# Performance work log

Hardware: AMD Instinct MI355X
Metric: run time of the kernel (lower is better)

The kernel has to match this reference:

```python
import jax, jax.numpy as jnp
import numpy as np
import math

B, Q, D = 1, 1024, 4096
H, KV, HD = 32, 8, 128
GROUP_FACTOR, LABEL_BITS, HEAVY_CONST = 8, 4, 256
ROPE_THETA = 10000.0
NEG = jnp.finfo(jnp.float32).min


def setup_inputs() -> dict:
    key = jax.random.key(0)
    ks = jax.random.split(key, 5)
    hidden_states = jax.random.normal(ks[0], (B, Q, D), jnp.float32)
    Wq = jax.random.normal(ks[1], (D, H * HD), jnp.float32) * 0.02
    Wk = jax.random.normal(ks[2], (D, KV * HD), jnp.float32) * 0.02
    Wv = jax.random.normal(ks[3], (D, KV * HD), jnp.float32) * 0.02
    Wo = jax.random.normal(ks[4], (H * HD, D), jnp.float32) * 0.02
    # additive causal mask [B,1,Q,Q]
    causal = jnp.tril(jnp.ones((Q, Q), bool))
    attention_mask = jnp.where(causal, 0.0, NEG)[None, None].astype(jnp.float32)
    position_ids = jnp.arange(Q, dtype=jnp.int64 if jax.config.jax_enable_x64 else jnp.int32)[None]
    # per-head channel permutation (sorted channel importance order)
    rng = np.random.default_rng(0)
    sorted_channel = jnp.asarray(np.stack([rng.permutation(HD) for _ in range(H)]), jnp.int32)
    return {"hidden_states": hidden_states, "attention_mask": attention_mask,
            "position_ids": position_ids, "Wq": Wq, "Wk": Wk, "Wv": Wv, "Wo": Wo,
            "sorted_channel": sorted_channel}


def pseudo_quantize(t, q_bit):
    max_quant = 2 ** q_bit - 1
    mn = jnp.min(t, axis=-1, keepdims=True)
    mx = jnp.max(t, axis=-1, keepdims=True)
    rng = mx - mn
    rng = jnp.where(rng == 0, 1.0, rng)
    scale = max_quant / rng
    quant = jnp.clip(jnp.round((t - mn) * scale), 0, max_quant)
    return quant / scale + mn


def rotate_half(x):
    x1, x2 = jnp.split(x, 2, axis=-1)
    return jnp.concatenate([-x2, x1], axis=-1)


def _forward(hidden_states, attention_mask, Wq, Wk, Wv, Wo, position_ids, sorted_channel):
    bsz, q_len, _ = hidden_states.shape
    q = (hidden_states @ Wq).reshape(bsz, q_len, H, HD).transpose(0, 2, 1, 3)   # [B,H,Q,HD]
    k = (hidden_states @ Wk).reshape(bsz, q_len, KV, HD).transpose(0, 2, 1, 3)  # [B,KV,Q,HD]
    v = (hidden_states @ Wv).reshape(bsz, q_len, KV, HD).transpose(0, 2, 1, 3)
    kv_len = q_len

    # RoPE
    inv_freq = 1.0 / (ROPE_THETA ** (jnp.arange(0, HD, 2, dtype=jnp.float32) / HD))
    freqs = position_ids.astype(jnp.float32)[..., None] * inv_freq  # [B,Q,HD/2]
    emb = jnp.concatenate([freqs, freqs], axis=-1)
    cos = jnp.cos(emb)[:, None]  # [B,1,Q,HD]
    sin = jnp.sin(emb)[:, None]
    q = q * cos + rotate_half(q) * sin
    k = k * cos + rotate_half(k) * sin
    prev_q = q  # upper_layer_embedding is None -> previous_query_states == query_states

    # GQA repeat
    groups = H // KV
    k = jnp.repeat(k, groups, axis=1)  # [B,H,K,HD]
    v = jnp.repeat(v, groups, axis=1)

    attn = jnp.einsum('bhqd,bhkd->bhqk', q, k) / math.sqrt(HD)

    # channel gather per head (sorted_channel: [H,HD] permutation)
    idx = jnp.broadcast_to(sorted_channel[None, :, None, :], q.shape)
    sq = jnp.take_along_axis(prev_q, idx, axis=-1)
    sk = jnp.take_along_axis(k, jnp.broadcast_to(sorted_channel[None, :, None, :], k.shape), axis=-1)
    outlier = HD // GROUP_FACTOR
    gq = sq[..., :outlier]
    gk = sk[..., :outlier]
    if LABEL_BITS < 16:
        gq = pseudo_quantize(gq, LABEL_BITS)
        gk = pseudo_quantize(gk, LABEL_BITS)
    gattn = jnp.einsum('bhqd,bhkd->bhqk', gq, gk) / math.sqrt(outlier)

    attn = attn + attention_mask
    gattn = gattn + attention_mask

    # keep top heavy_const positions per query by grouped score (descending)
    rank = jnp.argsort(jnp.argsort(-gattn, axis=-1), axis=-1)
    attn = jnp.where(rank < HEAVY_CONST, attn, -jnp.inf)

    w = jax.nn.softmax(attn.astype(jnp.float32), axis=-1).astype(v.dtype)
    out = jnp.einsum('bhqk,bhkd->bhqd', w, v)
    out = out.transpose(0, 2, 1, 3).reshape(bsz, q_len, H * HD)
    return out @ Wo


def reference(hidden_states, attention_mask, position_ids, Wq, Wk, Wv, Wo, sorted_channel):
    return _forward(hidden_states, attention_mask, Wq, Wk, Wv, Wo, position_ids, sorted_channel)
```

## Files before the change

### kernel.cpp

```cpp
#include <hip/hip_runtime.h>
#include <hip/hip_bf16.h>
#include <math.h>


typedef __hip_bfloat16 bf16;
typedef unsigned short ushort_t;
typedef __attribute__((ext_vector_type(8))) short short8;
typedef __attribute__((ext_vector_type(4))) float f32x4;
typedef __attribute__((ext_vector_type(4))) unsigned u32x4;

#define QL   1024
#define DM   4096
#define NH   32
#define NKV  8
#define GRP  4
#define HD   128
#define OUTL 16
#define HC   256
#define MNEG (-1.0e30f)

__device__ __forceinline__ unsigned mapf(float f) {
  unsigned u = __float_as_uint(f);
  return (u & 0x80000000u) ? ~u : (u | 0x80000000u);
}

__device__ __forceinline__ unsigned short f2bf(float x) {
  unsigned u = __float_as_uint(x);
  unsigned r = (u + 0x7FFFu + ((u >> 16) & 1u)) >> 16;
  return (unsigned short)r;
}
__device__ __forceinline__ float bf2f(unsigned short h) {
  return __uint_as_float(((unsigned)h) << 16);
}

__device__ __forceinline__ void split8(const float* p, short8& h, short8& l) {
  f32x4 a = *(const f32x4*)p;
  f32x4 b = *(const f32x4*)(p + 4);
#pragma unroll
  for (int i = 0; i < 4; i++) {
    unsigned short hh = f2bf(a[i]);
    h[i] = (short)hh;
    l[i] = (short)f2bf(a[i] - bf2f(hh));
  }
#pragma unroll
  for (int i = 0; i < 4; i++) {
    unsigned short hh = f2bf(b[i]);
    h[4 + i] = (short)hh;
    l[4 + i] = (short)f2bf(b[i] - bf2f(hh));
  }
}

__device__ __forceinline__ void splitp8(const float* p, unsigned* o) {
  f32x4 a = *(const f32x4*)p;
  f32x4 b = *(const f32x4*)(p + 4);
#pragma unroll
  for (int i = 0; i < 4; i++) {
    unsigned short hh = f2bf(a[i]);
    unsigned short ll = f2bf(a[i] - bf2f(hh));
    o[i] = (unsigned)hh | ((unsigned)ll << 16);
  }
#pragma unroll
  for (int i = 0; i < 4; i++) {
    unsigned short hh = f2bf(b[i]);
    unsigned short ll = f2bf(b[i] - bf2f(hh));
    o[4 + i] = (unsigned)hh | ((unsigned)ll << 16);
  }
}

__device__ __forceinline__ int aswz(int r, int k) {
  return r * 32 + (k ^ (((r >> 1) & 3) << 3));
}

__device__ __forceinline__ void gll16(const bf16* g, bf16* l) {
  __builtin_amdgcn_global_load_lds(
      (const __attribute__((address_space(1))) void*)g,
      (__attribute__((address_space(3))) void*)l, 16, 0, 0);
}

__device__ __forceinline__ int s4(int col) {
  return col ^ (((col >> 5) & 7) << 2);
}

__device__ __forceinline__ int dppReduce32(int v) {
  v += __builtin_amdgcn_update_dpp(0, v, 0xB1, 0xF, 0xF, true);
  v += __builtin_amdgcn_update_dpp(0, v, 0x4E, 0xF, 0xF, true);
  v += __builtin_amdgcn_update_dpp(0, v, 0x124, 0xF, 0xF, true);
  v += __builtin_amdgcn_update_dpp(0, v, 0x128, 0xF, 0xF, true);
  v += __builtin_amdgcn_ds_swizzle(v, 0x401F);
  return v;
}

__global__ __launch_bounds__(256)
void transpose_bf16_kernel(const bf16* __restrict__ src, bf16* __restrict__ dst,
                           int K, int N, long long srcBS, long long dstBS) {
  __shared__ alignas(16) unsigned short tile[64][64];
  const bf16* s = src + (size_t)blockIdx.z * srcBS;
  bf16* d = dst + (size_t)blockIdx.z * dstBS;
  const int k0 = blockIdx.y * 64, n0 = blockIdx.x * 64;
  const int t = threadIdx.x;
  {
    const int r = t >> 3;
    const int c8 = (t & 7) * 8;
    const int sw0 = ((r >> 3) & 7) * 8;
    const int sw1 = (((r + 32) >> 3) & 7) * 8;
    *(short8*)&tile[r][c8 ^ sw0] =
        *(const short8*)&s[(size_t)(k0 + r) * N + n0 + c8];
    *(short8*)&tile[r + 32][c8 ^ sw1] =
        *(const short8*)&s[(size_t)(k0 + r + 32) * N + n0 + c8];
  }
  __syncthreads();
  {
    const int kc8 = t & 7;
    const int nr = t >> 3;
    short8 v0, v1;
#pragma unroll
    for (int j = 0; j < 8; j++) {
      const int rowj = kc8 * 8 + j;
      const int swj = ((rowj >> 3) & 7) * 8;
      v0[j] = (short)tile[rowj][nr ^ swj];
      v1[j] = (short)tile[rowj][(nr + 32) ^ swj];
    }
    *(short8*)&d[(size_t)(n0 + nr) * K + k0 + kc8 * 8] = v0;
    *(short8*)&d[(size_t)(n0 + nr + 32) * K + k0 + kc8 * 8] = v1;
  }
}

__global__ __launch_bounds__(256)
void split_a_kernel(const void* __restrict__ hsv, bf16* __restrict__ Ah,
                    bf16* __restrict__ Al, const ushort_t* __restrict__ msk) {
  const bool ibf = (msk[1] != 0);
  const int gid = blockIdx.x * 256 + threadIdx.x;
  const int m = gid >> 9, c = gid & 511;
  const int cs = c ^ ((m >> 1) & 3);
  const size_t srci = (size_t)m * DM + (size_t)c * 8;
  const size_t dsti = (size_t)m * DM + (size_t)cs * 8;
  if (ibf) {
    *(short8*)&Ah[dsti] = *(const short8*)((const bf16*)hsv + srci);
  } else {
    short8 h, l;
    split8((const float*)hsv + srci, h, l);
    *(short8*)&Ah[dsti] = h;
    *(short8*)&Al[dsti] = l;
  }
}

__global__ __launch_bounds__(256)
void wsplitT_kernel(const void* __restrict__ src, int Nsrc,
                    bf16* __restrict__ dh, bf16* __restrict__ dl,
                    int n_off, int wantLo, const ushort_t* __restrict__ msk) {
  const bool ibf = (msk[1] != 0);
  __shared__ alignas(16) unsigned tile[64][64];
  const int n0 = blockIdx.x * 64;
  const int k0 = blockIdx.y * 64;
  const int t = threadIdx.x;
  {
    const int r = t >> 3, c8 = (t & 7) * 8;
    unsigned p0[8], p1[8];
    if (ibf) {
      const bf16* S = (const bf16*)src;
      short8 v0 = *(const short8*)&S[(size_t)(k0 + r) * Nsrc + n0 + c8];
      short8 v1 = *(const short8*)&S[(size_t)(k0 + r + 32) * Nsrc + n0 + c8];
#pragma unroll
      for (int i = 0; i < 8; i++) {
        p0[i] = (unsigned)(unsigned short)v0[i];
        p1[i] = (unsigned)(unsigned short)v1[i];
      }
    } else {
      const float* S = (const float*)src;
      splitp8(&S[(size_t)(k0 + r) * Nsrc + n0 + c8], p0);
      splitp8(&S[(size_t)(k0 + r + 32) * Nsrc + n0 + c8], p1);
    }
    const int sw0 = ((r >> 3) & 7) * 8;
    const int sw1 = (((r + 32) >> 3) & 7) * 8;
    *(u32x4*)&tile[r][c8 ^ sw0] = *(u32x4*)&p0[0];
    *(u32x4*)&tile[r][(c8 ^ sw0) + 4] = *(u32x4*)&p0[4];
    *(u32x4*)&tile[r + 32][c8 ^ sw1] = *(u32x4*)&p1[0];
    *(u32x4*)&tile[r + 32][(c8 ^ sw1) + 4] = *(u32x4*)&p1[4];
  }
  __syncthreads();
  {
    const int kc8 = t & 7, nr = t >> 3;
    short8 h0, l0, h1, l1;
#pragma unroll
    for (int j = 0; j < 8; j++) {
      const int rowj = kc8 * 8 + j;
      const int swj = ((rowj >> 3) & 7) * 8;
      unsigned g0 = tile[rowj][nr ^ swj];
      unsigned g1 = tile[rowj][(nr + 32) ^ swj];
      h0[j] = (short)(g0 & 0xFFFFu); l0[j] = (short)(g0 >> 16);
      h1[j] = (short)(g1 & 0xFFFFu); l1[j] = (short)(g1 >> 16);
    }
    const int na = n_off + n0 + nr, nb = na + 32;
    const int cha = (k0 >> 3) + (kc8 ^ ((na >> 1) & 3));
    const int chb = (k0 >> 3) + (kc8 ^ ((nb >> 1) & 3));
    *(short8*)&dh[(size_t)na * DM + ((size_t)cha << 3)] = h0;
    *(short8*)&dh[(size_t)nb * DM + ((size_t)chb << 3)] = h1;
    if (wantLo && !ibf) {
      *(short8*)&dl[(size_t)na * DM + ((size_t)cha << 3)] = l0;
      *(short8*)&dl[(size_t)nb * DM + ((size_t)chb << 3)] = l1;
    }
  }
}

__global__ __launch_bounds__(256)
void gemm_qkv2_kernel(const bf16* __restrict__ Ah, const bf16* __restrict__ Al,
                      const bf16* __restrict__ WhT, const bf16* __restrict__ WlT,
                      float* __restrict__ C, const ushort_t* __restrict__ msk) {
  const bool ibf = (msk[1] != 0);
  const int n0 = blockIdx.x * 128;
  const int m0 = blockIdx.y * 64;
  const bool doSplit = (n0 < 5120) && !ibf;

  __shared__ alignas(16) bf16 sAh[64 * 32];
  __shared__ alignas(16) bf16 sAl[64 * 32];
  __shared__ alignas(16) bf16 sBh[128 * 32];
  __shared__ alignas(16) bf16 sBl[128 * 32];

  const int t = threadIdx.x, lane = t & 63, wave = t >> 6;
  const int wm = (wave >> 1) * 32, wn = (wave & 1) * 64;
  const int mrow = lane & 15, kq = (lane >> 4) * 8;
  const size_t aoff = (size_t)(m0 + (t >> 2)) * DM + (size_t)(t & 3) * 8;
  const size_t boff0 = (size_t)(n0 + (t >> 2)) * DM + (size_t)(t & 3) * 8;
  const size_t boff1 = (size_t)(n0 + 64 + (t >> 2)) * DM + (size_t)(t & 3) * 8;
  bf16* lA_h = sAh + wave * 512;
  bf16* lA_l = sAl + wave * 512;
  bf16* lB0h = sBh + wave * 512;
  bf16* lB1h = sBh + 2048 + wave * 512;
  bf16* lB0l = sBl + wave * 512;
  bf16* lB1l = sBl + 2048 + wave * 512;

  f32x4 acc[2][4];
#pragma unroll
  for (int i = 0; i < 2; i++)
#pragma unroll
    for (int j = 0; j < 4; j++) acc[i][j] = (f32x4){0.f, 0.f, 0.f, 0.f};

  for (int kk = 0; kk < DM; kk += 32) {
    __syncthreads();
    gll16(Ah + aoff + kk, lA_h);
    gll16(WhT + boff0 + kk, lB0h);
    gll16(WhT + boff1 + kk, lB1h);
    if (doSplit) {
      gll16(Al + aoff + kk, lA_l);
      gll16(WlT + boff0 + kk, lB0l);
      gll16(WlT + boff1 + kk, lB1l);
    }
    __syncthreads();
    short8 afh[2], bfh[4];
#pragma unroll
    for (int i = 0; i < 2; i++)
      afh[i] = *(const short8*)&sAh[aswz(wm + i * 16 + mrow, kq)];
#pragma unroll
    for (int j = 0; j < 4; j++)
      bfh[j] = *(const short8*)&sBh[aswz(wn + j * 16 + mrow, kq)];
#pragma unroll
    for (int i = 0; i < 2; i++)
#pragma unroll
      for (int j = 0; j < 4; j++)
        acc[i][j] = __builtin_amdgcn_mfma_f32_16x16x32_bf16(afh[i], bfh[j], acc[i][j], 0, 0, 0);
    if (doSplit) {
      short8 afl[2], bfl[4];
#pragma unroll
      for (int i = 0; i < 2; i++)
        afl[i] = *(const short8*)&sAl[aswz(wm + i * 16 + mrow, kq)];
#pragma unroll
      for (int j = 0; j < 4; j++)
        bfl[j] = *(const short8*)&sBl[aswz(wn + j * 16 + mrow, kq)];
#pragma unroll
      for (int i = 0; i < 2; i++)
#pragma unroll
        for (int j = 0; j < 4; j++) {
          acc[i][j] = __builtin_amdgcn_mfma_f32_16x16x32_bf16(afh[i], bfl[j], acc[i][j], 0, 0, 0);
          acc[i][j] = __builtin_amdgcn_mfma_f32_16x16x32_bf16(afl[i], bfh[j], acc[i][j], 0, 0, 0);
        }
    }
  }
  const int rq = (lane >> 4) * 4, cn = lane & 15;
#pragma unroll
  for (int i = 0; i < 2; i++)
#pragma unroll
    for (int r = 0; r < 4; r++) {
      const size_t rowi = (size_t)(m0 + wm + i * 16 + rq + r);
#pragma unroll
      for (int j = 0; j < 4; j++)
        C[rowi * 6144 + (n0 + wn + j * 16 + cn)] = acc[i][j][r];
    }
}

__global__ __launch_bounds__(256)
void gemm_wo2_kernel(const bf16* __restrict__ Ao, const bf16* __restrict__ WoT,
                     void* __restrict__ Cv, const ushort_t* __restrict__ msk) {
  const bool ibf = (msk[1] != 0);
  __shared__ alignas(16) bf16 sA[64 * 32];
  __shared__ alignas(16) bf16 sB[128 * 32];
  const int n0 = blockIdx.x * 128;
  const int m0 = blockIdx.y * 64;
  const int t = threadIdx.x, lane = t & 63, wave = t >> 6;
  const int wm = (wave >> 1) * 32, wn = (wave & 1) * 64;
  const int mrow = lane & 15, kq = (lane >> 4) * 8;
  const size_t aoff = (size_t)(m0 + (t >> 2)) * DM + (size_t)(t & 3) * 8;
  const size_t boff0 = (size_t)(n0 + (t >> 2)) * DM + (size_t)(t & 3) * 8;
  const size_t boff1 = (size_t)(n0 + 64 + (t >> 2)) * DM + (size_t)(t & 3) * 8;
  bf16* lA = sA + wave * 512;
  bf16* lB0 = sB + wave * 512;
  bf16* lB1 = sB + 2048 + wave * 512;

  f32x4 acc[2][4];
#pragma unroll
  for (int i = 0; i < 2; i++)
#pragma unroll
    for (int j = 0; j < 4; j++) acc[i][j] = (f32x4){0.f, 0.f, 0.f, 0.f};

  for (int kk = 0; kk < DM; kk += 32) {
    __syncthreads();
    gll16(Ao + aoff + kk, lA);
    gll16(WoT + boff0 + kk, lB0);
    gll16(WoT + boff1 + kk, lB1);
    __syncthreads();
    short8 af[2], bfr[4];
#pragma unroll
    for (int i = 0; i < 2; i++)
      af[i] = *(const short8*)&sA[aswz(wm + i * 16 + mrow, kq)];
#pragma unroll
    for (int j = 0; j < 4; j++)
      bfr[j] = *(const short8*)&sB[aswz(wn + j * 16 + mrow, kq)];
#pragma unroll
    for (int i = 0; i < 2; i++)
#pragma unroll
      for (int j = 0; j < 4; j++)
        acc[i][j] = __builtin_amdgcn_mfma_f32_16x16x32_bf16(af[i], bfr[j], acc[i][j], 0, 0, 0);
  }
  const int rq = (lane >> 4) * 4, cn = lane & 15;
#pragma unroll
  for (int i = 0; i < 2; i++)
#pragma unroll
    for (int r = 0; r < 4; r++) {
      const size_t rowi = (size_t)(m0 + wm + i * 16 + rq + r);
#pragma unroll
      for (int j = 0; j < 4; j++) {
        const size_t idx = rowi * DM + (n0 + wn + j * 16 + cn);
        if (ibf)
          ((bf16*)Cv)[idx] = __float2bfloat16(acc[i][j][r]);
        else
          ((float*)Cv)[idx] = acc[i][j][r];
      }
    }
}

__global__ __launch_bounds__(128)
void rope_cs_kernel(float* __restrict__ cs, float* __restrict__ sn) {
  const int pos = blockIdx.x, d = threadIdx.x;
  const float inv = (float)(1.0 / pow(10000.0, (double)(d & 63) * (1.0 / 64.0)));
  const float ang = (float)pos * inv;
  cs[pos * HD + d] = cosf(ang);
  sn[pos * HD + d] = sinf(ang);
}

__global__ __launch_bounds__(128)
void rope_q_gq_kernel(const float* __restrict__ qkv, const int* __restrict__ sc,
                      bf16* __restrict__ qr, float* __restrict__ gq,
                      const float* __restrict__ cs, const float* __restrict__ sn) {
  const int pos = blockIdx.x, h = blockIdx.y, d = threadIdx.x;
  __shared__ float sv[HD], sr[HD];
  __shared__ float smn, smx;
  float v = qkv[(size_t)pos * 6144 + h * HD + d];
  sv[d] = v;
  __syncthreads();
  const float c = cs[pos * HD + d], s = sn[pos * HD + d];
  float rot = (d < 64) ? -sv[d + 64] : sv[d - 64];
  float r = v * c + rot * s;
  sr[d] = r;
  qr[((size_t)h * QL + pos) * HD + d] = __float2bfloat16(r);
  __syncthreads();
  if (d == 0) {
    float mn = 3.4e38f, mx = -3.4e38f;
    for (int j = 0; j < OUTL; j++) {
      float g = sr[sc[h * HD + j]];
      mn = fminf(mn, g);
      mx = fmaxf(mx, g);
    }
    smn = mn; smx = mx;
  }
  __syncthreads();
  if (d < OUTL) {
    float g = sr[sc[h * HD + d]];
    float rng = smx - smn;
    if (rng == 0.f) rng = 1.f;
    float scale = 15.0f / rng;
    float qv = rintf((g - smn) * scale);
    qv = fminf(fmaxf(qv, 0.f), 15.f);
    gq[((size_t)h * QL + pos) * OUTL + d] = qv / scale + smn;
  }
}

__global__ __launch_bounds__(128)
void rope_k_gk_kernel(const float* __restrict__ qkv, const int* __restrict__ sc,
                      bf16* __restrict__ kr, bf16* __restrict__ vrow,
                      float* __restrict__ gk,
                      const float* __restrict__ cs, const float* __restrict__ sn) {
  const int pos = blockIdx.x, kvh = blockIdx.y, d = threadIdx.x;
  __shared__ float sv[HD], sr[HD];
  __shared__ float smn[GRP], smx[GRP];
  float kv = qkv[(size_t)pos * 6144 + DM + kvh * HD + d];
  float vv = qkv[(size_t)pos * 6144 + DM + NKV * HD + kvh * HD + d];
  sv[d] = kv;
  __syncthreads();
  const float c = cs[pos * HD + d], s = sn[pos * HD + d];
  float rot = (d < 64) ? -sv[d + 64] : sv[d - 64];
  float r = kv * c + rot * s;
  sr[d] = r;
  kr[((size_t)kvh * QL + pos) * HD + d] = __float2bfloat16(r);
  vrow[((size_t)kvh * QL + pos) * HD + d] = __float2bfloat16(vv);
  __syncthreads();
  if (d < 64 && (d & 15) == 0) {
    const int g = d >> 4;
    const int h = kvh * GRP + g;
    float mn = 3.4e38f, mx = -3.4e38f;
    for (int j = 0; j < OUTL; j++) {
      float x = sr[sc[h * HD + j]];
      mn = fminf(mn, x);
      mx = fmaxf(mx, x);
    }
    smn[g] = mn; smx[g] = mx;
  }
  __syncthreads();
  if (d < 64) {
    const int g = d >> 4, j = d & 15;
    const int h = kvh * GRP + g;
    float x = sr[sc[h * HD + j]];
    float rng = smx[g] - smn[g];
    if (rng == 0.f) rng = 1.f;
    float scale = 15.0f / rng;
    float qv = rintf((x - smn[g]) * scale);
    qv = fminf(fmaxf(qv, 0.f), 15.f);
    gk[((size_t)h * QL + pos) * OUTL + j] = qv / scale + smn[g];
  }
}

__global__ __launch_bounds__(256)
void attn_kernel(const bf16* __restrict__ qr, const bf16* __restrict__ kr,
                 const bf16* __restrict__ vT, const float* __restrict__ gq,
                 const float* __restrict__ gk, bf16* __restrict__ ao) {
  const int h = blockIdx.y;
  const int q0 = ((int)gridDim.x - 1 - (int)blockIdx.x) * 8;
  const int kvh = h >> 2;
  const int t = threadIdx.x;
  const int lane = t & 63, wave = t >> 6;
  const int mrow = lane & 15, kq = (lane >> 4) * 8;
  const int row = t >> 5, j32 = t & 31;
  const int kmax = q0 + 8;
  const bool needSel = (kmax > HC);

  __shared__ alignas(16) bf16 sQ[16][HD];
  __shared__ float sGq[8][OUTL];
  __shared__ alignas(16) float sBuf[8][QL];
  __shared__ float sL[8];

  {
    const int r = t >> 4, c8 = (t & 15) * 8;
    short8 z = {0, 0, 0, 0, 0, 0, 0, 0};
    if (r < 8)
      *(short8*)&sQ[r][c8] = *(const short8*)&qr[((size_t)h * QL + q0 + r) * HD + c8];
    else
      *(short8*)&sQ[r][c8] = z;
    if (needSel && t < 128)
      sGq[t >> 4][t & 15] = gq[((size_t)h * QL + q0 + (t >> 4)) * OUTL + (t & 15)];
  }
  __syncthreads();

  unsigned sel = 0xFFFFFFFFu;
  if (needSel) {
    for (int kk = t; kk < kmax; kk += 256) {
      const float* gkp = &gk[((size_t)h * QL + kk) * OUTL];
      float gv[OUTL];
#pragma unroll
      for (int j = 0; j < OUTL; j++) gv[j] = gkp[j];
      const int pk = s4(kk);
#pragma unroll
      for (int r = 0; r < 8; r++) {
        float s = 0.f;
#pragma unroll
        for (int j = 0; j < OUTL; j++) s += sGq[r][j] * gv[j];
        sBuf[r][pk] = (kk <= q0 + r) ? s * 0.25f : MNEG;
      }
    }
    __syncthreads();

    {
      const int base = j32 * 32;
      const int cz = j32 & 7;
      unsigned uv[32];
#pragma unroll
      for (int g = 0; g < 8; g++) {
        f32x4 v = *(const f32x4*)&sBuf[row][base + ((g ^ cz) << 2)];
#pragma unroll
        for (int m = 0; m < 4; m++) {
          const int kk = g * 4 + m;
          uv[kk] = (base + kk < kmax) ? mapf(v[m]) : 0u;
        }
      }
#define TST(J, M)                                                     \
  _Pragma("unroll") for (int k2 = 0; k2 < 32; k2++) if ((k2 & (J)) == 0) { \
    unsigned tt = (uv[k2] ^ (uv[k2 + (J)] >> (J))) & (M);             \
    uv[k2] ^= tt;                                                     \
    uv[k2 + (J)] ^= (tt << (J));                                      \
  }
      TST(16, 0x0000FFFFu)
      TST(8, 0x00FF00FFu)
      TST(4, 0x0F0F0F0Fu)
      TST(2, 0x33333333u)
      TST(1, 0x55555555u)
#undef TST
      unsigned act = 0xFFFFFFFFu, gtm = 0u;
      int greater = 0, act_tot = QL;
      bool done = false;
#pragma unroll
      for (int p = 0; p < 32; p++) {
        if (__all(done)) break;
        if (!done) {
          const unsigned ones = act & uv[p];
          const int c = dppReduce32(__popc(ones));
          if (greater + c >= HC) {
            act = ones;
            act_tot = c;
          } else {
            greater += c;
            gtm |= ones;
            act ^= ones;
            act_tot -= c;
          }
          if (greater + act_tot == HC) {
            sel = __brev(gtm | act);
            done = true;
          }
        }
      }
      if (!done) {
        const unsigned gtmN = __brev(gtm), eqmN = __brev(act);
        const int needEq = HC - greater;
        const int eqc = __popc(eqmN);
        int pre = eqc;
#pragma unroll
        for (int dlt = 1; dlt < 32; dlt <<= 1) {
          int o = __shfl_up(pre, dlt, 32);
          if (j32 >= dlt) pre += o;
        }
        pre -= eqc;
        int take = needEq - pre;
        unsigned mm = eqmN;
        sel = gtmN;
        for (int i = 0; i < take && mm != 0u; i++) {
          unsigned b = mm & (0u - mm);
          sel |= b;
          mm ^= b;
        }
      }
    }
    __syncthreads();
  }

  {
    short8 aq[4];
#pragma unroll
    for (int kb = 0; kb < 4; kb++)
      aq[kb] = *(const short8*)&sQ[mrow][kb * 32 + kq];
    const bf16* krh = &kr[(size_t)kvh * QL * HD];
    const int ntmax = (kmax + 15) >> 4;
    for (int nt = wave; nt < ntmax; nt += 4) {
      const int kb0 = nt * 16;
      f32x4 acc = {0.f, 0.f, 0.f, 0.f};
#pragma unroll
      for (int kb = 0; kb < 4; kb++) {
        short8 bfr = *(const short8*)&krh[(size_t)(kb0 + mrow) * HD + kb * 32 + kq];
        acc = __builtin_amdgcn_mfma_f32_16x16x32_bf16(aq[kb], bfr, acc, 0, 0, 0);
      }
      const int key = kb0 + mrow;
      const int pk = s4(key);
#pragma unroll
      for (int r = 0; r < 4; r++) {
        const int m = (lane >> 4) * 4 + r;
        if (m < 8) {
          float v = acc[r] * 0.08838834764831845f;
          sBuf[m][pk] = (key <= q0 + m) ? v : MNEG;
        }
      }
    }
  }
  __syncthreads();

  const int kbmax = (kmax + 31) >> 5;

  {
    const int base = j32 * 32;
    const int cz = j32 & 7;
    const int rbound = q0 + row;
    float av[32];
#pragma unroll
    for (int g = 0; g < 8; g++) {
      f32x4 v = *(const f32x4*)&sBuf[row][base + ((g ^ cz) << 2)];
#pragma unroll
      for (int m = 0; m < 4; m++) av[g * 4 + m] = v[m];
    }
    float mx = MNEG;
#pragma unroll
    for (int kk = 0; kk < 32; kk++)
      if (((sel >> kk) & 1u) && (base + kk <= rbound)) mx = fmaxf(mx, av[kk]);
    mx = fmaxf(mx, __shfl_xor(mx, 1, 32));
    mx = fmaxf(mx, __shfl_xor(mx, 2, 32));
    mx = fmaxf(mx, __shfl_xor(mx, 4, 32));
    mx = fmaxf(mx, __shfl_xor(mx, 8, 32));
    mx = fmaxf(mx, __shfl_xor(mx, 16, 32));
    float ls = 0.f;
#pragma unroll
    for (int kk = 0; kk < 32; kk++) {
      float p = 0.f;
      if (((sel >> kk) & 1u) && (base + kk <= rbound)) {
        float e = av[kk] - mx;
        p = (e < -80.f) ? 0.f : expf(e);
        ls += p;
      }
      av[kk] = p;
    }
    ls += __shfl_xor(ls, 1, 32);
    ls += __shfl_xor(ls, 2, 32);
    ls += __shfl_xor(ls, 4, 32);
    ls += __shfl_xor(ls, 8, 32);
    ls += __shfl_xor(ls, 16, 32);
    if (j32 == 0) sL[row] = ls;
    __syncthreads();
    bf16* P = (bf16*)&sBuf[0][0];
    if (j32 < kbmax) {
      const int rk = row & 3;
#pragma unroll
      for (int g = 0; g < 4; g++) {
        short8 pv8;
#pragma unroll
        for (int m = 0; m < 8; m++) pv8[m] = (short)f2bf(av[g * 8 + m]);
        *(short8*)&P[(size_t)row * QL + base + ((g ^ rk) << 3)] = pv8;
      }
    }
    {
      const int zr = 8 + row;
      if (j32 < kbmax) {
        short8 z = {0, 0, 0, 0, 0, 0, 0, 0};
#pragma unroll
        for (int i = 0; i < 4; i++)
          *(short8*)&P[(size_t)zr * QL + j32 * 32 + i * 8] = z;
      }
    }
  }
  __syncthreads();

  {
    const bf16* Pb = (const bf16*)&sBuf[0][0];
    const bf16* vTh = &vT[(size_t)kvh * HD * QL];
    const int rk = mrow & 3;
    for (int dt = wave; dt < 8; dt += 4) {
      const int d0 = dt * 16;
      f32x4 acc = {0.f, 0.f, 0.f, 0.f};
      for (int kb = 0; kb < kbmax; kb++) {
        short8 af = *(const short8*)&Pb[(size_t)mrow * QL + kb * 32 + (kq ^ (rk << 3))];
        short8 bfr = *(const short8*)&vTh[(size_t)(d0 + mrow) * QL + kb * 32 + kq];
        acc = __builtin_amdgcn_mfma_f32_16x16x32_bf16(af, bfr, acc, 0, 0, 0);
      }
#pragma unroll
      for (int r = 0; r < 4; r++) {
        const int m = (lane >> 4) * 4 + r;
        if (m < 8) {
          float outv = acc[r] / sL[m];
          const int rowm = q0 + m;
          const int col = h * HD + d0 + mrow;
          const int ch = (col >> 3) ^ ((rowm >> 1) & 3);
          ao[(size_t)rowm * DM + (ch << 3) + (col & 7)] = __float2bfloat16(outv);
        }
      }
    }
  }
}

extern "C" void kernel_launch(void* const* d_in, const int* in_sizes, int n_in,
                              void* d_out, int out_size, void* d_ws, size_t ws_size,
                              hipStream_t stream) {
  (void)in_sizes; (void)n_in; (void)out_size; (void)ws_size;
  const void* hs = d_in[0];
  const ushort_t* msk = (const ushort_t*)d_in[1];
  const void* Wq = d_in[3];
  const void* Wk = d_in[4];
  const void* Wv = d_in[5];
  const void* Wo = d_in[6];
  const int* sc = (const int*)d_in[7];

  char* ws = (char*)d_ws;
  size_t off = 0;
  auto alloc = [&](size_t bytes) {
    char* p = ws + off;
    off += (bytes + 255) & ~(size_t)255;
    return p;
  };
  float* qkv = (float*)alloc((size_t)QL * 6144 * 4);
  bf16* ao = (bf16*)qkv;
  bf16* qr = (bf16*)alloc((size_t)NH * QL * HD * 2);
  bf16* kr = (bf16*)alloc((size_t)NKV * QL * HD * 2);
  bf16* vrow = (bf16*)alloc((size_t)NKV * QL * HD * 2);
  bf16* vT = (bf16*)alloc((size_t)NKV * HD * QL * 2);
  float* gq = (float*)alloc((size_t)NH * QL * OUTL * 4);
  float* gk = (float*)alloc((size_t)NH * QL * OUTL * 4);
  float* cst = (float*)alloc((size_t)QL * HD * 4);
  float* snt = (float*)alloc((size_t)QL * HD * 4);
  bf16* Ahs = (bf16*)alloc((size_t)QL * DM * 2);
  bf16* Als = (bf16*)alloc((size_t)QL * DM * 2);
  bf16* WhT = (bf16*)alloc((size_t)6144 * DM * 2);
  bf16* WlT = (bf16*)alloc((size_t)5120 * DM * 2);
  bf16* WoT = WhT;

  rope_cs_kernel<<<dim3(QL), 128, 0, stream>>>(cst, snt);

  split_a_kernel<<<dim3(2048), 256, 0, stream>>>(hs, Ahs, Als, msk);
  wsplitT_kernel<<<dim3(64, 64), 256, 0, stream>>>(Wq, 4096, WhT, WlT, 0, 1, msk);
  wsplitT_kernel<<<dim3(16, 64), 256, 0, stream>>>(Wk, 1024, WhT, WlT, 4096, 1, msk);
  wsplitT_kernel<<<dim3(16, 64), 256, 0, stream>>>(Wv, 1024, WhT, WlT, 5120, 0, msk);

  gemm_qkv2_kernel<<<dim3(48, 16), 256, 0, stream>>>(Ahs, Als, WhT, WlT, qkv, msk);

  rope_q_gq_kernel<<<dim3(QL, NH), 128, 0, stream>>>(qkv, sc, qr, gq, cst, snt);
  rope_k_gk_kernel<<<dim3(QL, NKV), 128, 0, stream>>>(qkv, sc, kr, vrow, gk, cst, snt);
  transpose_bf16_kernel<<<dim3(2, 16, NKV), 256, 0, stream>>>(
      vrow, vT, QL, HD, (long long)(QL * HD), (long long)(HD * QL));

  wsplitT_kernel<<<dim3(64, 64), 256, 0, stream>>>(Wo, 4096, WoT, WlT, 0, 0, msk);
  attn_kernel<<<dim3(QL / 8, NH), 256, 0, stream>>>(qr, kr, vT, gq, gk, ao);

  gemm_wo2_kernel<<<dim3(32, 16), 256, 0, stream>>>(ao, WoT, d_out, msk);
}
```

Baseline: 626.8 us.

## Restructure attention kernel to 16-row tiles with paired causal halves

The attention kernel now processes 16 query rows per tile instead of 8, so the MFMA 16-row dimension is fully used rather than half padded with zeros. Each block handles two tiles from opposite ends of the causal range to balance work, and the grid shrinks to 32 blocks per head. The grouped-score top-k selection is computed straight into registers per thread instead of through a shared-memory buffer. QK scores are staged through a smaller swizzled buffer in windows of 256 keys, with two extra barriers per window. It also uses packed bf16 conversion and a launch-bounds occupancy hint, at the cost of more registers per thread and repeated gk reads across threads.

```diff
diff --git a/kernel.cpp b/kernel.cpp
--- a/kernel.cpp
+++ b/kernel.cpp
@@ -33,6 +33,12 @@
   return __uint_as_float(((unsigned)h) << 16);
 }
 
+__device__ __forceinline__ unsigned cvtpk(float a, float b) {
+  unsigned r;
+  asm("v_cvt_pk_bf16_f32 %0, %1, %2" : "=v"(r) : "v"(a), "v"(b));
+  return r;
+}
+
 __device__ __forceinline__ void split8(const float* p, short8& h, short8& l) {
   f32x4 a = *(const f32x4*)p;
   f32x4 b = *(const f32x4*)(p + 4);
@@ -77,8 +83,16 @@
       (__attribute__((address_space(3))) void*)l, 16, 0, 0);
 }
 
-__device__ __forceinline__ int s4(int col) {
-  return col ^ (((col >> 5) & 7) << 2);
+__device__ __forceinline__ int pswz(int r, int c) {
+  return r * 1024 + (c ^ ((((r & 7) ^ ((c >> 5) & 7)) & 7) << 3));
+}
+
+__device__ __forceinline__ int sswz(int m, int k) {
+  return m * 260 + (k ^ (((k >> 5) & 7) << 2));
+}
+
+__device__ __forceinline__ int qswz(int r, int c) {
+  return r * HD + (c ^ ((r & 7) << 3));
 }
 
 __device__ __forceinline__ int dppReduce32(int v) {
@@ -88,6 +102,98 @@
   v += __builtin_amdgcn_update_dpp(0, v, 0x128, 0xF, 0xF, true);
   v += __builtin_amdgcn_ds_swizzle(v, 0x401F);
   return v;
+}
+
+__device__ __forceinline__ unsigned topkSel(unsigned (&uv)[32], int j32) {
+#define TST(J, M)                                                     \
+  _Pragma("unroll") for (int k2 = 0; k2 < 32; k2++) if ((k2 & (J)) == 0) { \
+    unsigned tt = (uv[k2] ^ (uv[k2 + (J)] >> (J))) & (M);             \
+    uv[k2] ^= tt;                                                     \
+    uv[k2 + (J)] ^= (tt << (J));                                      \
+  }
+  TST(16, 0x0000FFFFu)
+  TST(8, 0x00FF00FFu)
+  TST(4, 0x0F0F0F0Fu)
+  TST(2, 0x33333333u)
+  TST(1, 0x55555555u)
+#undef TST
+  unsigned sel = 0xFFFFFFFFu;
+  unsigned act = 0xFFFFFFFFu, gtm = 0u;
+  int greater = 0, act_tot = QL;
+  bool done = false;
+#pragma unroll
+  for (int p = 0; p < 32; p++) {
+    if (__all(done)) break;
+    if (!done) {
+      const unsigned ones = act & uv[p];
+      const int c = dppReduce32(__popc(ones));
+      if (greater + c >= HC) {
+        act = ones;
+        act_tot = c;
+      } else {
+        greater += c;
+        gtm |= ones;
+        act ^= ones;
+        act_tot -= c;
+      }
+      if (greater + act_tot == HC) {
+        sel = __brev(gtm | act);
+        done = true;
+      }
+    }
+  }
+  if (!done) {
+    const unsigned gtmN = __brev(gtm), eqmN = __brev(act);
+    const int needEq = HC - greater;
+    const int eqc = __popc(eqmN);
+    int pre = eqc;
+#pragma unroll
+    for (int dlt = 1; dlt < 32; dlt <<= 1) {
+      int o = __shfl_up(pre, dlt, 32);
+      if (j32 >= dlt) pre += o;
+    }
+    pre -= eqc;
+    int take = needEq - pre;
+    unsigned mm = eqmN;
+    sel = gtmN;
+    for (int i = 0; i < take && mm != 0u; i++) {
+      unsigned b = mm & (0u - mm);
+      sel |= b;
+      mm ^= b;
+    }
+  }
+  return sel;
+}
+
+__device__ __forceinline__ unsigned gattnSel(const float* __restrict__ gqrow,
+                                             const float* __restrict__ gkh,
+                                             int j32, int q0, int r, int kmax) {
+  float gqr[OUTL];
+#pragma unroll
+  for (int c = 0; c < 4; c++) {
+    f32x4 v = *(const f32x4*)(gqrow + 4 * c);
+#pragma unroll
+    for (int i = 0; i < 4; i++) gqr[4 * c + i] = v[i];
+  }
+  unsigned uv[32];
+#pragma unroll
+  for (int kk = 0; kk < 32; kk++) {
+    const int key = j32 * 32 + kk;
+    unsigned u = 0u;
+    if (key < kmax) {
+      const float* gp = gkh + (size_t)key * OUTL;
+      float s = 0.f;
+#pragma unroll
+      for (int c = 0; c < 4; c++) {
+        f32x4 v = *(const f32x4*)(gp + 4 * c);
+#pragma unroll
+        for (int i = 0; i < 4; i++) s += gqr[4 * c + i] * v[i];
+      }
+      u = mapf((key <= q0 + r) ? s * 0.25f : MNEG);
+    }
+    uv[kk] = u;
+  }
+  return topkSel(uv, j32);
 }
 
 __global__ __launch_bounds__(256)
@@ -437,236 +543,158 @@
   }
 }
 
-__global__ __launch_bounds__(256)
+__global__ __launch_bounds__(256, 4)
 void attn_kernel(const bf16* __restrict__ qr, const bf16* __restrict__ kr,
                  const bf16* __restrict__ vT, const float* __restrict__ gq,
                  const float* __restrict__ gk, bf16* __restrict__ ao) {
   const int h = blockIdx.y;
-  const int q0 = ((int)gridDim.x - 1 - (int)blockIdx.x) * 8;
+  const int xb = blockIdx.x;
   const int kvh = h >> 2;
   const int t = threadIdx.x;
   const int lane = t & 63, wave = t >> 6;
   const int mrow = lane & 15, kq = (lane >> 4) * 8;
-  const int row = t >> 5, j32 = t & 31;
-  const int kmax = q0 + 8;
-  const bool needSel = (kmax > HC);
-
-  __shared__ alignas(16) bf16 sQ[16][HD];
-  __shared__ float sGq[8][OUTL];
-  __shared__ alignas(16) float sBuf[8][QL];
-  __shared__ float sL[8];
-
-  {
-    const int r = t >> 4, c8 = (t & 15) * 8;
-    short8 z = {0, 0, 0, 0, 0, 0, 0, 0};
-    if (r < 8)
-      *(short8*)&sQ[r][c8] = *(const short8*)&qr[((size_t)h * QL + q0 + r) * HD + c8];
-    else
-      *(short8*)&sQ[r][c8] = z;
-    if (needSel && t < 128)
-      sGq[t >> 4][t & 15] = gq[((size_t)h * QL + q0 + (t >> 4)) * OUTL + (t & 15)];
-  }
-  __syncthreads();
-
-  unsigned sel = 0xFFFFFFFFu;
-  if (needSel) {
-    for (int kk = t; kk < kmax; kk += 256) {
-      const float* gkp = &gk[((size_t)h * QL + kk) * OUTL];
-      float gv[OUTL];
-#pragma unroll
-      for (int j = 0; j < OUTL; j++) gv[j] = gkp[j];
-      const int pk = s4(kk);
-#pragma unroll
-      for (int r = 0; r < 8; r++) {
-        float s = 0.f;
-#pragma unroll
-        for (int j = 0; j < OUTL; j++) s += sGq[r][j] * gv[j];
-        sBuf[r][pk] = (kk <= q0 + r) ? s * 0.25f : MNEG;
-      }
-    }
+  const int g = t >> 5, j32 = t & 31;
+  const int r0 = g, r1 = g + 8;
+
+  __shared__ alignas(16) bf16 sQ[16 * HD];
+  __shared__ alignas(16) char sMem[16 * 1024 * 2];
+  __shared__ float sL[16];
+  bf16* sP = (bf16*)sMem;
+  float* stg = (float*)sMem;
+
+  const float* gkh = &gk[(size_t)h * QL * OUTL];
+  const bf16* krh = &kr[(size_t)kvh * QL * HD];
+  const bf16* vTh = &vT[(size_t)kvh * HD * QL];
+
+  for (int half = 0; half < 2; half++) {
+    const int q0 = (half == 0) ? (63 - xb) * 16 : xb * 16;
+    const int kmax = q0 + 16;
+    const bool needSel = (kmax > HC);
     __syncthreads();
 
     {
-      const int base = j32 * 32;
-      const int cz = j32 & 7;
-      unsigned uv[32];
-#pragma unroll
-      for (int g = 0; g < 8; g++) {
-        f32x4 v = *(const f32x4*)&sBuf[row][base + ((g ^ cz) << 2)];
-#pragma unroll
-        for (int m = 0; m < 4; m++) {
-          const int kk = g * 4 + m;
-          uv[kk] = (base + kk < kmax) ? mapf(v[m]) : 0u;
-        }
-      }
-#define TST(J, M)                                                     \
-  _Pragma("unroll") for (int k2 = 0; k2 < 32; k2++) if ((k2 & (J)) == 0) { \
-    unsigned tt = (uv[k2] ^ (uv[k2 + (J)] >> (J))) & (M);             \
-    uv[k2] ^= tt;                                                     \
-    uv[k2 + (J)] ^= (tt << (J));                                      \
-  }
-      TST(16, 0x0000FFFFu)
-      TST(8, 0x00FF00FFu)
-      TST(4, 0x0F0F0F0Fu)
-      TST(2, 0x33333333u)
-      TST(1, 0x55555555u)
-#undef TST
-      unsigned act = 0xFFFFFFFFu, gtm = 0u;
-      int greater = 0, act_tot = QL;
-      bool done = false;
-#pragma unroll
-      for (int p = 0; p < 32; p++) {
-        if (__all(done)) break;
-        if (!done) {
-          const unsigned ones = act & uv[p];
-          const int c = dppReduce32(__popc(ones));
-          if (greater + c >= HC) {
-            act = ones;
-            act_tot = c;
-          } else {
-            greater += c;
-            gtm |= ones;
-            act ^= ones;
-            act_tot -= c;
+      const int r = t >> 4, c8 = (t & 15) * 8;
+      *(short8*)&sQ[qswz(r, c8)] =
+          *(const short8*)&qr[((size_t)h * QL + q0 + r) * HD + c8];
+    }
+
+    unsigned sela = 0xFFFFFFFFu, selb = 0xFFFFFFFFu;
+    if (needSel) {
+      sela = gattnSel(&gq[((size_t)h * QL + q0 + r0) * OUTL], gkh, j32, q0, r0, kmax);
+      selb = gattnSel(&gq[((size_t)h * QL + q0 + r1) * OUTL], gkh, j32, q0, r1, kmax);
+    }
+    __syncthreads();
+
+    float ava[32], avb[32];
+    {
+      short8 aq[4];
+#pragma unroll
+      for (int kb = 0; kb < 4; kb++)
+        aq[kb] = *(const short8*)&sQ[qswz(mrow, kb * 32 + kq)];
+      const int ntmax = kmax >> 4;
+      const int nw = (ntmax + 15) >> 4;
+      for (int w = 0; w < nw; w++) {
+        const int ntend = (w * 16 + 16 < ntmax) ? (w * 16 + 16) : ntmax;
+        for (int nt = w * 16 + wave; nt < ntend; nt += 4) {
+          const int kb0 = nt * 16;
+          f32x4 acc = {0.f, 0.f, 0.f, 0.f};
+#pragma unroll
+          for (int kb = 0; kb < 4; kb++) {
+            short8 bfr = *(const short8*)&krh[(size_t)(kb0 + mrow) * HD + kb * 32 + kq];
+            acc = __builtin_amdgcn_mfma_f32_16x16x32_bf16(aq[kb], bfr, acc, 0, 0, 0);
           }
-          if (greater + act_tot == HC) {
-            sel = __brev(gtm | act);
-            done = true;
+          const int key = kb0 + mrow;
+          const int keyp = key & 255;
+#pragma unroll
+          for (int r = 0; r < 4; r++) {
+            const int m = (lane >> 4) * 4 + r;
+            float v = acc[r] * 0.08838834764831845f;
+            stg[sswz(m, keyp)] = (key <= q0 + m) ? v : MNEG;
           }
         }
-      }
-      if (!done) {
-        const unsigned gtmN = __brev(gtm), eqmN = __brev(act);
-        const int needEq = HC - greater;
-        const int eqc = __popc(eqmN);
-        int pre = eqc;
-#pragma unroll
-        for (int dlt = 1; dlt < 32; dlt <<= 1) {
-          int o = __shfl_up(pre, dlt, 32);
-          if (j32 >= dlt) pre += o;
+        __syncthreads();
+        if ((j32 >> 3) == w) {
+          const int kb8 = (j32 & 7) * 32;
+#pragma unroll
+          for (int c = 0; c < 8; c++) {
+            f32x4 va = *(const f32x4*)&stg[sswz(r0, kb8 + 4 * c)];
+            f32x4 vb = *(const f32x4*)&stg[sswz(r1, kb8 + 4 * c)];
+#pragma unroll
+            for (int i = 0; i < 4; i++) {
+              ava[4 * c + i] = va[i];
+              avb[4 * c + i] = vb[i];
+            }
+          }
         }
-        pre -= eqc;
-        int take = needEq - pre;
-        unsigned mm = eqmN;
-        sel = gtmN;
-        for (int i = 0; i < take && mm != 0u; i++) {
-          unsigned b = mm & (0u - mm);
-          sel |= b;
-          mm ^= b;
+        __syncthreads();
+      }
+    }
+
+    {
+      const int rb0 = q0 + r0, rb1 = q0 + r1;
+      float mxa = MNEG, mxb = MNEG;
+#pragma unroll
+      for (int kk = 0; kk < 32; kk++) {
+        const int key = j32 * 32 + kk;
+        if (((sela >> kk) & 1u) && key <= rb0) mxa = fmaxf(mxa, ava[kk]);
+        if (((selb >> kk) & 1u) && key <= rb1) mxb = fmaxf(mxb, avb[kk]);
+      }
+#pragma unroll
+      for (int dlt = 1; dlt < 32; dlt <<= 1) {
+        mxa = fmaxf(mxa, __shfl_xor(mxa, dlt, 32));
+        mxb = fmaxf(mxb, __shfl_xor(mxb, dlt, 32));
+      }
+      float la = 0.f, lb = 0.f;
+#pragma unroll
+      for (int kk = 0; kk < 32; kk++) {
+        const int key = j32 * 32 + kk;
+        float pa = 0.f, pb = 0.f;
+        if (((sela >> kk) & 1u) && key <= rb0) {
+          float e = ava[kk] - mxa;
+          pa = (e < -80.f) ? 0.f : expf(e);
+          la += pa;
         }
+        if (((selb >> kk) & 1u) && key <= rb1) {
+          float e = avb[kk] - mxb;
+          pb = (e < -80.f) ? 0.f : expf(e);
+          lb += pb;
+        }
+        ava[kk] = pa;
+        avb[kk] = pb;
+      }
+#pragma unroll
+      for (int dlt = 1; dlt < 32; dlt <<= 1) {
+        la += __shfl_xor(la, dlt, 32);
+        lb += __shfl_xor(lb, dlt, 32);
+      }
+      if (j32 == 0) { sL[r0] = la; sL[r1] = lb; }
+#pragma unroll
+      for (int c = 0; c < 4; c++) {
+        u32x4 ua, ub;
+#pragma unroll
+        for (int i = 0; i < 4; i++) {
+          ua[i] = cvtpk(ava[c * 8 + 2 * i], ava[c * 8 + 2 * i + 1]);
+          ub[i] = cvtpk(avb[c * 8 + 2 * i], avb[c * 8 + 2 * i + 1]);
+        }
+        *(u32x4*)&sP[pswz(r0, j32 * 32 + c * 8)] = ua;
+        *(u32x4*)&sP[pswz(r1, j32 * 32 + c * 8)] = ub;
       }
     }
     __syncthreads();
-  }
-
-  {
-    short8 aq[4];
-#pragma unroll
-    for (int kb = 0; kb < 4; kb++)
-      aq[kb] = *(const short8*)&sQ[mrow][kb * 32 + kq];
-    const bf16* krh = &kr[(size_t)kvh * QL * HD];
-    const int ntmax = (kmax + 15) >> 4;
-    for (int nt = wave; nt < ntmax; nt += 4) {
-      const int kb0 = nt * 16;
-      f32x4 acc = {0.f, 0.f, 0.f, 0.f};
-#pragma unroll
-      for (int kb = 0; kb < 4; kb++) {
-        short8 bfr = *(const short8*)&krh[(size_t)(kb0 + mrow) * HD + kb * 32 + kq];
-        acc = __builtin_amdgcn_mfma_f32_16x16x32_bf16(aq[kb], bfr, acc, 0, 0, 0);
-      }
-      const int key = kb0 + mrow;
-      const int pk = s4(key);
-#pragma unroll
-      for (int r = 0; r < 4; r++) {
-        const int m = (lane >> 4) * 4 + r;
-        if (m < 8) {
-          float v = acc[r] * 0.08838834764831845f;
-          sBuf[m][pk] = (key <= q0 + m) ? v : MNEG;
+
+    {
+      const int kbmax = (kmax + 31) >> 5;
+      for (int dt = wave; dt < 8; dt += 4) {
+        const int d0 = dt * 16;
+        f32x4 acc = {0.f, 0.f, 0.f, 0.f};
+        for (int kb = 0; kb < kbmax; kb++) {
+          short8 af = *(const short8*)&sP[pswz(mrow, kb * 32 + kq)];
+          short8 bfr = *(const short8*)&vTh[(size_t)(d0 + mrow) * QL + kb * 32 + kq];
+          acc = __builtin_amdgcn_mfma_f32_16x16x32_bf16(af, bfr, acc, 0, 0, 0);
         }
-      }
-    }
-  }
-  __syncthreads();
-
-  const int kbmax = (kmax + 31) >> 5;
-
-  {
-    const int base = j32 * 32;
-    const int cz = j32 & 7;
-    const int rbound = q0 + row;
-    float av[32];
-#pragma unroll
-    for (int g = 0; g < 8; g++) {
-      f32x4 v = *(const f32x4*)&sBuf[row][base + ((g ^ cz) << 2)];
-#pragma unroll
-      for (int m = 0; m < 4; m++) av[g * 4 + m] = v[m];
-    }
-    float mx = MNEG;
-#pragma unroll
-    for (int kk = 0; kk < 32; kk++)
-      if (((sel >> kk) & 1u) && (base + kk <= rbound)) mx = fmaxf(mx, av[kk]);
-    mx = fmaxf(mx, __shfl_xor(mx, 1, 32));
-    mx = fmaxf(mx, __shfl_xor(mx, 2, 32));
-    mx = fmaxf(mx, __shfl_xor(mx, 4, 32));
-    mx = fmaxf(mx, __shfl_xor(mx, 8, 32));
-    mx = fmaxf(mx, __shfl_xor(mx, 16, 32));
-    float ls = 0.f;
-#pragma unroll
-    for (int kk = 0; kk < 32; kk++) {
-      float p = 0.f;
-      if (((sel >> kk) & 1u) && (base + kk <= rbound)) {
-        float e = av[kk] - mx;
-        p = (e < -80.f) ? 0.f : expf(e);
-        ls += p;
-      }
-      av[kk] = p;
-    }
-    ls += __shfl_xor(ls, 1, 32);
-    ls += __shfl_xor(ls, 2, 32);
-    ls += __shfl_xor(ls, 4, 32);
-    ls += __shfl_xor(ls, 8, 32);
-    ls += __shfl_xor(ls, 16, 32);
-    if (j32 == 0) sL[row] = ls;
-    __syncthreads();
-    bf16* P = (bf16*)&sBuf[0][0];
-    if (j32 < kbmax) {
-      const int rk = row & 3;
-#pragma unroll
-      for (int g = 0; g < 4; g++) {
-        short8 pv8;
-#pragma unroll
-        for (int m = 0; m < 8; m++) pv8[m] = (short)f2bf(av[g * 8 + m]);
-        *(short8*)&P[(size_t)row * QL + base + ((g ^ rk) << 3)] = pv8;
-      }
-    }
-    {
-      const int zr = 8 + row;
-      if (j32 < kbmax) {
-        short8 z = {0, 0, 0, 0, 0, 0, 0, 0};
-#pragma unroll
-        for (int i = 0; i < 4; i++)
-          *(short8*)&P[(size_t)zr * QL + j32 * 32 + i * 8] = z;
-      }
-    }
-  }
-  __syncthreads();
-
-  {
-    const bf16* Pb = (const bf16*)&sBuf[0][0];
-    const bf16* vTh = &vT[(size_t)kvh * HD * QL];
-    const int rk = mrow & 3;
-    for (int dt = wave; dt < 8; dt += 4) {
-      const int d0 = dt * 16;
-      f32x4 acc = {0.f, 0.f, 0.f, 0.f};
-      for (int kb = 0; kb < kbmax; kb++) {
-        short8 af = *(const short8*)&Pb[(size_t)mrow * QL + kb * 32 + (kq ^ (rk << 3))];
-        short8 bfr = *(const short8*)&vTh[(size_t)(d0 + mrow) * QL + kb * 32 + kq];
-        acc = __builtin_amdgcn_mfma_f32_16x16x32_bf16(af, bfr, acc, 0, 0, 0);
-      }
-#pragma unroll
-      for (int r = 0; r < 4; r++) {
-        const int m = (lane >> 4) * 4 + r;
-        if (m < 8) {
+#pragma unroll
+        for (int r = 0; r < 4; r++) {
+          const int m = (lane >> 4) * 4 + r;
           float outv = acc[r] / sL[m];
           const int rowm = q0 + m;
           const int col = h * HD + d0 + mrow;
@@ -728,7 +756,7 @@
       vrow, vT, QL, HD, (long long)(QL * HD), (long long)(HD * QL));
 
   wsplitT_kernel<<<dim3(64, 64), 256, 0, stream>>>(Wo, 4096, WoT, WlT, 0, 0, msk);
-  attn_kernel<<<dim3(QL / 8, NH), 256, 0, stream>>>(qr, kr, vT, gq, gk, ao);
+  attn_kernel<<<dim3(32, NH), 256, 0, stream>>>(qr, kr, vT, gq, gk, ao);
 
   gemm_wo2_kernel<<<dim3(32, 16), 256, 0, stream>>>(ao, WoT, d_out, msk);
 }
```

Measured after the change: 883.5 us. +41.0%, slower.
